# Performance work log

Measured on AMD Instinct MI355X. Metric: run time of the kernel, lower is better.

The kernel has to match this reference:

```python
import jax, jax.numpy as jnp
import numpy as np

B, N, D, C = 256, 256, 512, 1024
EPS = 1e-12  # F.normalize eps


def _l2norm(x):
    n = jnp.linalg.norm(x, axis=-1, keepdims=True)
    return x / jnp.maximum(n, EPS)


def setup_inputs() -> dict:
    key = jax.random.key(0)
    k1, k2, k3 = jax.random.split(key, 3)
    return {
        "image_tokens": jax.random.normal(k1, (B, N, D), dtype=jnp.float32),
        "text_features": jax.random.normal(k2, (C, D), dtype=jnp.float32),
        "log_tau": jnp.asarray(np.log(0.07), dtype=jnp.float32),
        "log_attn_tau": jnp.asarray(np.log(0.07), dtype=jnp.float32),
        "pid_labels": jax.random.randint(k3, (B,), 0, C),
    }


def reference(image_tokens, text_features, log_tau, log_attn_tau, pid_labels):
    toks = _l2norm(image_tokens.astype(jnp.float32))        # [B,N,D]
    txt = _l2norm(text_features.astype(jnp.float32))        # [C,D]
    sims = jnp.einsum('bnd,cd->bnc', toks, txt)             # [B,N,C]
    gt = pid_labels.astype(jnp.int32)
    # sims[arange(B), :, gt] -> [B,N]
    sims_gt = jnp.take_along_axis(sims, gt[:, None, None], axis=2)[..., 0]
    attn_tau = jnp.clip(jnp.exp(log_attn_tau), 0.01, 1.0)
    w = jax.nn.softmax(sims_gt / attn_tau, axis=1)          # [B,N]
    logits = jnp.einsum('bn,bnc->bc', w, sims)              # [B,C]
    tau = jnp.clip(jnp.exp(log_tau), 0.01, 1.0)
    logits = logits / tau
    # cross_entropy with label_smoothing=0.0, mean reduction
    logp = jax.nn.log_softmax(logits, axis=-1)
    nll = -jnp.take_along_axis(logp, gt[:, None], axis=1)[:, 0]
    return jnp.mean(nll)
```

## Files before the change

### kernel.cpp

```cpp
#include <hip/hip_runtime.h>
#include <math.h>

#define Bb 256
#define Nn 256
#define Dd 512
#define Cc 1024
#define KC 8
#define KD (Dd / KC)
#define BT 8

__device__ __forceinline__ float waveReduceSum(float v) {
    #pragma unroll
    for (int off = 32; off > 0; off >>= 1)
        v += __shfl_xor(v, off, 64);
    return v;
}
__device__ __forceinline__ float waveReduceMax(float v) {
    #pragma unroll
    for (int off = 32; off > 0; off >>= 1)
        v = fmaxf(v, __shfl_xor(v, off, 64));
    return v;
}

__global__ void __launch_bounds__(1024) k_attn_q(const float* __restrict__ toks,
                                                 const float* __restrict__ txt,
                                                 const int* __restrict__ pid,
                                                 const float* __restrict__ log_attn_tau,
                                                 float* __restrict__ q,
                                                 float* __restrict__ txt_t,
                                                 float* __restrict__ accf,
                                                 int* __restrict__ cnt) {
    const int b = blockIdx.x;
    const int tid = threadIdx.x;
    const int wv = tid >> 6;
    const int lane = tid & 63;
    __shared__ float xg[Dd];
    __shared__ float r8[8];
    __shared__ float tss[16];
    __shared__ float qpart_s[16][Dd];
    __shared__ float ms[16], Ss[16];

    if (b == 0 && tid == 0) { accf[0] = 0.0f; cnt[0] = 0; }

    const int g = pid[b];
    float v = 0.f;
    if (tid < Dd) v = txt[(size_t)g * Dd + tid];

    const int c0 = b * 4;
    const int row = tid >> 8;
    const int col2 = (tid & 255) * 2;
    const float2 tv = *(const float2*)&txt[(size_t)(c0 + row) * Dd + col2];

    float p = waveReduceSum(v * v);
    float ssp = waveReduceSum(tv.x * tv.x + tv.y * tv.y);
    if (lane == 0) { if (wv < 8) r8[wv] = p; tss[wv] = ssp; }
    __syncthreads();

    const float tot = r8[0]+r8[1]+r8[2]+r8[3]+r8[4]+r8[5]+r8[6]+r8[7];
    const float invg = 1.0f / fmaxf(sqrtf(tot), 1e-12f);
    if (tid < Dd) xg[tid] = v * invg;

    {
        const float rss = tss[4*row] + tss[4*row+1] + tss[4*row+2] + tss[4*row+3];
        const float invr = 1.0f / fmaxf(sqrtf(rss), 1e-12f);
        txt_t[(size_t)col2 * Cc + c0 + row] = tv.x * invr;
        txt_t[(size_t)(col2 + 1) * Cc + c0 + row] = tv.y * invr;
    }
    __syncthreads();

    float at = expf(log_attn_tau[0]);
    at = fminf(fmaxf(at, 0.01f), 1.0f);
    const float iat = 1.0f / at;

    const float4 xg0 = *(const float4*)&xg[lane * 8];
    const float4 xg1 = *(const float4*)&xg[lane * 8 + 4];

    float m = -INFINITY, S = 0.0f;
    float qa[8] = {0.f, 0.f, 0.f, 0.f, 0.f, 0.f, 0.f, 0.f};

    const float* base = toks + ((size_t)b * Nn + wv * 16) * Dd + (size_t)lane * 8;
    float4 c0v[4], c1v[4];
    #pragma unroll
    for (int k = 0; k < 4; ++k) {
        c0v[k] = *(const float4*)(base + k * Dd);
        c1v[k] = *(const float4*)(base + k * Dd + 4);
    }
    #pragma unroll
    for (int batch = 0; batch < 4; ++batch) {
        float4 n0[4], n1[4];
        if (batch < 3) {
            const float* pn = base + (batch + 1) * 4 * Dd;
            #pragma unroll
            for (int k = 0; k < 4; ++k) {
                n0[k] = *(const float4*)(pn + k * Dd);
                n1[k] = *(const float4*)(pn + k * Dd + 4);
            }
        }
        float dt[4], ss[4];
        #pragma unroll
        for (int k = 0; k < 4; ++k) {
            dt[k] = c0v[k].x*xg0.x + c0v[k].y*xg0.y + c0v[k].z*xg0.z + c0v[k].w*xg0.w
                  + c1v[k].x*xg1.x + c1v[k].y*xg1.y + c1v[k].z*xg1.z + c1v[k].w*xg1.w;
            ss[k] = c0v[k].x*c0v[k].x + c0v[k].y*c0v[k].y + c0v[k].z*c0v[k].z + c0v[k].w*c0v[k].w
                  + c1v[k].x*c1v[k].x + c1v[k].y*c1v[k].y + c1v[k].z*c1v[k].z + c1v[k].w*c1v[k].w;
        }
        #pragma unroll
        for (int off = 32; off > 0; off >>= 1) {
            #pragma unroll
            for (int k = 0; k < 4; ++k) {
                dt[k] += __shfl_xor(dt[k], off, 64);
                ss[k] += __shfl_xor(ss[k], off, 64);
            }
        }
        #pragma unroll
        for (int k = 0; k < 4; ++k) {
            const float inv = 1.0f / fmaxf(sqrtf(ss[k]), 1e-12f);
            const float s = dt[k] * inv;
            if (s > m) {
                const float sc = expf((m - s) * iat);
                S = S * sc + 1.0f;
                qa[0] = qa[0]*sc + inv*c0v[k].x; qa[1] = qa[1]*sc + inv*c0v[k].y;
                qa[2] = qa[2]*sc + inv*c0v[k].z; qa[3] = qa[3]*sc + inv*c0v[k].w;
                qa[4] = qa[4]*sc + inv*c1v[k].x; qa[5] = qa[5]*sc + inv*c1v[k].y;
                qa[6] = qa[6]*sc + inv*c1v[k].z; qa[7] = qa[7]*sc + inv*c1v[k].w;
                m = s;
            } else {
                const float e = expf((s - m) * iat);
                S += e;
                const float w = e * inv;
                qa[0] = fmaf(w, c0v[k].x, qa[0]); qa[1] = fmaf(w, c0v[k].y, qa[1]);
                qa[2] = fmaf(w, c0v[k].z, qa[2]); qa[3] = fmaf(w, c0v[k].w, qa[3]);
                qa[4] = fmaf(w, c1v[k].x, qa[4]); qa[5] = fmaf(w, c1v[k].y, qa[5]);
                qa[6] = fmaf(w, c1v[k].z, qa[6]); qa[7] = fmaf(w, c1v[k].w, qa[7]);
            }
        }
        #pragma unroll
        for (int k = 0; k < 4; ++k) { c0v[k] = n0[k]; c1v[k] = n1[k]; }
    }
    #pragma unroll
    for (int j = 0; j < 8; ++j) qpart_s[wv][lane * 8 + j] = qa[j];
    if (lane == 0) { ms[wv] = m; Ss[wv] = S; }
    __syncthreads();
    if (tid < Dd) {
        float M = -INFINITY;
        #pragma unroll
        for (int w = 0; w < 16; ++w) M = fmaxf(M, ms[w]);
        float Stot = 0.f, acc = 0.f;
        #pragma unroll
        for (int w = 0; w < 16; ++w) {
            const float sc = expf((ms[w] - M) * iat);
            Stot = fmaf(Ss[w], sc, Stot);
            acc = fmaf(qpart_s[w][tid], sc, acc);
        }
        q[(size_t)b * Dd + tid] = acc / Stot;
    }
}

__global__ void k_logits(const float* __restrict__ q, const float* __restrict__ txt_t,
                         float* __restrict__ part) {
    const int b0 = blockIdx.x * BT;
    const int kc = blockIdx.y;
    const int d0 = kc * KD;
    const int t = threadIdx.x;
    __shared__ float qs[BT][KD];
    for (int i = t; i < BT * KD; i += 256)
        qs[i >> 6][i & 63] = q[(size_t)(b0 + (i >> 6)) * Dd + d0 + (i & 63)];
    __syncthreads();
    const float4* xt = (const float4*)txt_t;
    float4 a[BT];
    #pragma unroll
    for (int j = 0; j < BT; ++j) a[j] = make_float4(0.f, 0.f, 0.f, 0.f);
    #pragma unroll 2
    for (int d = 0; d < KD; d += 4) {
        const float4 x0 = xt[(size_t)(d0 + d + 0) * (Cc / 4) + t];
        const float4 x1 = xt[(size_t)(d0 + d + 1) * (Cc / 4) + t];
        const float4 x2 = xt[(size_t)(d0 + d + 2) * (Cc / 4) + t];
        const float4 x3 = xt[(size_t)(d0 + d + 3) * (Cc / 4) + t];
        #pragma unroll
        for (int j = 0; j < BT; ++j) {
            const float4 qj = *(const float4*)&qs[j][d];
            a[j].x = fmaf(qj.x,x0.x,a[j].x); a[j].y = fmaf(qj.x,x0.y,a[j].y); a[j].z = fmaf(qj.x,x0.z,a[j].z); a[j].w = fmaf(qj.x,x0.w,a[j].w);
            a[j].x = fmaf(qj.y,x1.x,a[j].x); a[j].y = fmaf(qj.y,x1.y,a[j].y); a[j].z = fmaf(qj.y,x1.z,a[j].z); a[j].w = fmaf(qj.y,x1.w,a[j].w);
            a[j].x = fmaf(qj.z,x2.x,a[j].x); a[j].y = fmaf(qj.z,x2.y,a[j].y); a[j].z = fmaf(qj.z,x2.z,a[j].z); a[j].w = fmaf(qj.z,x2.w,a[j].w);
            a[j].x = fmaf(qj.w,x3.x,a[j].x); a[j].y = fmaf(qj.w,x3.y,a[j].y); a[j].z = fmaf(qj.w,x3.z,a[j].z); a[j].w = fmaf(qj.w,x3.w,a[j].w);
        }
    }
    float* pb = part + ((size_t)kc * Bb + b0) * Cc;
    #pragma unroll
    for (int j = 0; j < BT; ++j) ((float4*)(pb + (size_t)j * Cc))[t] = a[j];
}

__global__ void k_lse_mean(const float* __restrict__ part, const int* __restrict__ pid,
                           const float* __restrict__ log_tau,
                           float* __restrict__ accf, int* __restrict__ cnt,
                           float* __restrict__ out) {
    const int b = blockIdx.x;
    const int t = threadIdx.x;
    float4 l = {0,0,0,0};
    #pragma unroll
    for (int kc = 0; kc < KC; ++kc) {
        const float4 p = ((const float4*)(part + ((size_t)kc * Bb + b) * Cc))[t];
        l.x += p.x; l.y += p.y; l.z += p.z; l.w += p.w;
    }
    float tau = expf(log_tau[0]);
    tau = fminf(fmaxf(tau, 0.01f), 1.0f);
    const float itau = 1.0f / tau;
    l.x *= itau; l.y *= itau; l.z *= itau; l.w *= itau;

    const int g = pid[b];
    __shared__ float redm[4], reds[4], sgt;
    if ((g >> 2) == t) {
        const float v[4] = {l.x, l.y, l.z, l.w};
        sgt = v[g & 3];
    }
    float m = fmaxf(fmaxf(l.x, l.y), fmaxf(l.z, l.w));
    m = waveReduceMax(m);
    if ((t & 63) == 0) redm[t >> 6] = m;
    __syncthreads();
    m = fmaxf(fmaxf(redm[0], redm[1]), fmaxf(redm[2], redm[3]));
    float e = expf(l.x - m) + expf(l.y - m) + expf(l.z - m) + expf(l.w - m);
    e = waveReduceSum(e);
    if ((t & 63) == 0) reds[t >> 6] = e;
    __syncthreads();
    if (t == 0) {
        const float S = reds[0] + reds[1] + reds[2] + reds[3];
        const float my = (m + logf(S) - sgt) * (1.0f / (float)Bb);
        atomicAdd(accf, my);
        __threadfence();
        const int c = atomicAdd(cnt, 1);
        if (c == Bb - 1) {
            out[0] = atomicAdd(accf, 0.0f);
        }
    }
}

extern "C" void kernel_launch(void* const* d_in, const int* in_sizes, int n_in,
                              void* d_out, int out_size, void* d_ws, size_t ws_size,
                              hipStream_t stream) {
    const float* toks = (const float*)d_in[0];
    const float* txt = (const float*)d_in[1];
    const float* log_tau = (const float*)d_in[2];
    const float* log_attn_tau = (const float*)d_in[3];
    const int* pid = (const int*)d_in[4];
    float* out = (float*)d_out;

    float* ws = (float*)d_ws;
    float* txt_t = ws;
    float* q     = txt_t + (size_t)Dd * Cc;
    float* part  = q + (size_t)Bb * Dd;
    float* accf  = part + (size_t)KC * Bb * Cc;
    int*   cnt   = (int*)(accf + 1);

    k_attn_q<<<Bb, 1024, 0, stream>>>(toks, txt, pid, log_attn_tau, q, txt_t, accf, cnt);
    k_logits<<<dim3(Bb / BT, KC), 256, 0, stream>>>(q, txt_t, part);
    k_lse_mean<<<Bb, 256, 0, stream>>>(part, pid, log_tau, accf, cnt, out);
}
```

Before: 220.9 us.

## Fuse three kernels into one cooperative kernel with grid syncs

Measured after the change: 311.0 us. +40.8%, slower.

```diff
diff --git a/kernel.cpp b/kernel.cpp
--- a/kernel.cpp
+++ b/kernel.cpp
@@ -1,4 +1,5 @@
 #include <hip/hip_runtime.h>
+#include <hip/hip_cooperative_groups.h>
 #include <math.h>
 
 #define Bb 256
@@ -9,6 +10,8 @@
 #define KD (Dd / KC)
 #define BT 8
 
+namespace cg = cooperative_groups;
+
 __device__ __forceinline__ float waveReduceSum(float v) {
     #pragma unroll
     for (int off = 32; off > 0; off >>= 1)
@@ -22,215 +25,211 @@
     return v;
 }
 
-__global__ void __launch_bounds__(1024) k_attn_q(const float* __restrict__ toks,
-                                                 const float* __restrict__ txt,
-                                                 const int* __restrict__ pid,
-                                                 const float* __restrict__ log_attn_tau,
-                                                 float* __restrict__ q,
-                                                 float* __restrict__ txt_t,
-                                                 float* __restrict__ accf,
-                                                 int* __restrict__ cnt) {
-    const int b = blockIdx.x;
+__global__ void __launch_bounds__(1024, 1) k_fused(
+    const float* __restrict__ toks, const float* __restrict__ txt,
+    const int* __restrict__ pid, const float* __restrict__ log_attn_tau,
+    const float* __restrict__ log_tau,
+    float* __restrict__ q, float* __restrict__ txt_t,
+    float* __restrict__ part, float* __restrict__ nll, float* __restrict__ out)
+{
+    cg::grid_group grid = cg::this_grid();
+    const int bid = blockIdx.x;
     const int tid = threadIdx.x;
     const int wv = tid >> 6;
     const int lane = tid & 63;
+
     __shared__ float xg[Dd];
     __shared__ float r8[8];
     __shared__ float tss[16];
     __shared__ float qpart_s[16][Dd];
     __shared__ float ms[16], Ss[16];
-
-    if (b == 0 && tid == 0) { accf[0] = 0.0f; cnt[0] = 0; }
-
-    const int g = pid[b];
-    float v = 0.f;
-    if (tid < Dd) v = txt[(size_t)g * Dd + tid];
-
-    const int c0 = b * 4;
-    const int row = tid >> 8;
-    const int col2 = (tid & 255) * 2;
-    const float2 tv = *(const float2*)&txt[(size_t)(c0 + row) * Dd + col2];
-
-    float p = waveReduceSum(v * v);
-    float ssp = waveReduceSum(tv.x * tv.x + tv.y * tv.y);
-    if (lane == 0) { if (wv < 8) r8[wv] = p; tss[wv] = ssp; }
-    __syncthreads();
-
-    const float tot = r8[0]+r8[1]+r8[2]+r8[3]+r8[4]+r8[5]+r8[6]+r8[7];
-    const float invg = 1.0f / fmaxf(sqrtf(tot), 1e-12f);
-    if (tid < Dd) xg[tid] = v * invg;
+    __shared__ float sgt_s;
 
     {
-        const float rss = tss[4*row] + tss[4*row+1] + tss[4*row+2] + tss[4*row+3];
-        const float invr = 1.0f / fmaxf(sqrtf(rss), 1e-12f);
-        txt_t[(size_t)col2 * Cc + c0 + row] = tv.x * invr;
-        txt_t[(size_t)(col2 + 1) * Cc + c0 + row] = tv.y * invr;
-    }
-    __syncthreads();
-
-    float at = expf(log_attn_tau[0]);
-    at = fminf(fmaxf(at, 0.01f), 1.0f);
-    const float iat = 1.0f / at;
-
-    const float4 xg0 = *(const float4*)&xg[lane * 8];
-    const float4 xg1 = *(const float4*)&xg[lane * 8 + 4];
-
-    float m = -INFINITY, S = 0.0f;
-    float qa[8] = {0.f, 0.f, 0.f, 0.f, 0.f, 0.f, 0.f, 0.f};
-
-    const float* base = toks + ((size_t)b * Nn + wv * 16) * Dd + (size_t)lane * 8;
-    float4 c0v[4], c1v[4];
-    #pragma unroll
-    for (int k = 0; k < 4; ++k) {
-        c0v[k] = *(const float4*)(base + k * Dd);
-        c1v[k] = *(const float4*)(base + k * Dd + 4);
-    }
-    #pragma unroll
-    for (int batch = 0; batch < 4; ++batch) {
-        float4 n0[4], n1[4];
-        if (batch < 3) {
-            const float* pn = base + (batch + 1) * 4 * Dd;
+        const int b = bid;
+        const int g = pid[b];
+        float v = 0.f;
+        if (tid < Dd) v = txt[(size_t)g * Dd + tid];
+
+        const int c0 = b * 4;
+        const int row = tid >> 8;
+        const int col2 = (tid & 255) * 2;
+        const float2 tv = *(const float2*)&txt[(size_t)(c0 + row) * Dd + col2];
+
+        float p = waveReduceSum(v * v);
+        float ssp = waveReduceSum(tv.x * tv.x + tv.y * tv.y);
+        if (lane == 0) { if (wv < 8) r8[wv] = p; tss[wv] = ssp; }
+        __syncthreads();
+
+        const float tot = r8[0]+r8[1]+r8[2]+r8[3]+r8[4]+r8[5]+r8[6]+r8[7];
+        const float invg = 1.0f / fmaxf(sqrtf(tot), 1e-12f);
+        if (tid < Dd) xg[tid] = v * invg;
+
+        {
+            const float rss = tss[4*row] + tss[4*row+1] + tss[4*row+2] + tss[4*row+3];
+            const float invr = 1.0f / fmaxf(sqrtf(rss), 1e-12f);
+            txt_t[(size_t)col2 * Cc + c0 + row] = tv.x * invr;
+            txt_t[(size_t)(col2 + 1) * Cc + c0 + row] = tv.y * invr;
+        }
+        __syncthreads();
+
+        float at = expf(log_attn_tau[0]);
+        at = fminf(fmaxf(at, 0.01f), 1.0f);
+        const float iat = 1.0f / at;
+
+        const float4 xg0 = *(const float4*)&xg[lane * 8];
+        const float4 xg1 = *(const float4*)&xg[lane * 8 + 4];
+
+        float m = -INFINITY, S = 0.0f;
+        float qa[8] = {0.f, 0.f, 0.f, 0.f, 0.f, 0.f, 0.f, 0.f};
+
+        const float* base = toks + ((size_t)b * Nn + wv * 16) * Dd + (size_t)lane * 8;
+        float4 c0v[4], c1v[4];
+        #pragma unroll
+        for (int k = 0; k < 4; ++k) {
+            c0v[k] = *(const float4*)(base + k * Dd);
+            c1v[k] = *(const float4*)(base + k * Dd + 4);
+        }
+        #pragma unroll
+        for (int batch = 0; batch < 4; ++batch) {
+            float4 n0[4], n1[4];
+            if (batch < 3) {
+                const float* pn = base + (batch + 1) * 4 * Dd;
+                #pragma unroll
+                for (int k = 0; k < 4; ++k) {
+                    n0[k] = *(const float4*)(pn + k * Dd);
+                    n1[k] = *(const float4*)(pn + k * Dd + 4);
+                }
+            }
+            float dt[4], ss[4];
             #pragma unroll
             for (int k = 0; k < 4; ++k) {
-                n0[k] = *(const float4*)(pn + k * Dd);
-                n1[k] = *(const float4*)(pn + k * Dd + 4);
-            }
-        }
-        float dt[4], ss[4];
-        #pragma unroll
-        for (int k = 0; k < 4; ++k) {
-            dt[k] = c0v[k].x*xg0.x + c0v[k].y*xg0.y + c0v[k].z*xg0.z + c0v[k].w*xg0.w
-                  + c1v[k].x*xg1.x + c1v[k].y*xg1.y + c1v[k].z*xg1.z + c1v[k].w*xg1.w;
-            ss[k] = c0v[k].x*c0v[k].x + c0v[k].y*c0v[k].y + c0v[k].z*c0v[k].z + c0v[k].w*c0v[k].w
-                  + c1v[k].x*c1v[k].x + c1v[k].y*c1v[k].y + c1v[k].z*c1v[k].z + c1v[k].w*c1v[k].w;
-        }
-        #pragma unroll
-        for (int off = 32; off > 0; off >>= 1) {
+                dt[k] = c0v[k].x*xg0.x + c0v[k].y*xg0.y + c0v[k].z*xg0.z + c0v[k].w*xg0.w
+                      + c1v[k].x*xg1.x + c1v[k].y*xg1.y + c1v[k].z*xg1.z + c1v[k].w*xg1.w;
+                ss[k] = c0v[k].x*c0v[k].x + c0v[k].y*c0v[k].y + c0v[k].z*c0v[k].z + c0v[k].w*c0v[k].w
+                      + c1v[k].x*c1v[k].x + c1v[k].y*c1v[k].y + c1v[k].z*c1v[k].z + c1v[k].w*c1v[k].w;
+            }
+            #pragma unroll
+            for (int off = 32; off > 0; off >>= 1) {
+                #pragma unroll
+                for (int k = 0; k < 4; ++k) {
+                    dt[k] += __shfl_xor(dt[k], off, 64);
+                    ss[k] += __shfl_xor(ss[k], off, 64);
+                }
+            }
             #pragma unroll
             for (int k = 0; k < 4; ++k) {
-                dt[k] += __shfl_xor(dt[k], off, 64);
-                ss[k] += __shfl_xor(ss[k], off, 64);
-            }
-        }
-        #pragma unroll
-        for (int k = 0; k < 4; ++k) {
-            const float inv = 1.0f / fmaxf(sqrtf(ss[k]), 1e-12f);
-            const float s = dt[k] * inv;
-            if (s > m) {
-                const float sc = expf((m - s) * iat);
-                S = S * sc + 1.0f;
-                qa[0] = qa[0]*sc + inv*c0v[k].x; qa[1] = qa[1]*sc + inv*c0v[k].y;
-                qa[2] = qa[2]*sc + inv*c0v[k].z; qa[3] = qa[3]*sc + inv*c0v[k].w;
-                qa[4] = qa[4]*sc + inv*c1v[k].x; qa[5] = qa[5]*sc + inv*c1v[k].y;
-                qa[6] = qa[6]*sc + inv*c1v[k].z; qa[7] = qa[7]*sc + inv*c1v[k].w;
-                m = s;
-            } else {
-                const float e = expf((s - m) * iat);
-                S += e;
-                const float w = e * inv;
-                qa[0] = fmaf(w, c0v[k].x, qa[0]); qa[1] = fmaf(w, c0v[k].y, qa[1]);
-                qa[2] = fmaf(w, c0v[k].z, qa[2]); qa[3] = fmaf(w, c0v[k].w, qa[3]);
-                qa[4] = fmaf(w, c1v[k].x, qa[4]); qa[5] = fmaf(w, c1v[k].y, qa[5]);
-                qa[6] = fmaf(w, c1v[k].z, qa[6]); qa[7] = fmaf(w, c1v[k].w, qa[7]);
-            }
-        }
-        #pragma unroll
-        for (int k = 0; k < 4; ++k) { c0v[k] = n0[k]; c1v[k] = n1[k]; }
-    }
-    #pragma unroll
-    for (int j = 0; j < 8; ++j) qpart_s[wv][lane * 8 + j] = qa[j];
-    if (lane == 0) { ms[wv] = m; Ss[wv] = S; }
-    __syncthreads();
-    if (tid < Dd) {
+                const float inv = 1.0f / fmaxf(sqrtf(ss[k]), 1e-12f);
+                const float s = dt[k] * inv;
+                if (s > m) {
+                    const float sc = expf((m - s) * iat);
+                    S = S * sc + 1.0f;
+                    qa[0] = qa[0]*sc + inv*c0v[k].x; qa[1] = qa[1]*sc + inv*c0v[k].y;
+                    qa[2] = qa[2]*sc + inv*c0v[k].z; qa[3] = qa[3]*sc + inv*c0v[k].w;
+                    qa[4] = qa[4]*sc + inv*c1v[k].x; qa[5] = qa[5]*sc + inv*c1v[k].y;
+                    qa[6] = qa[6]*sc + inv*c1v[k].z; qa[7] = qa[7]*sc + inv*c1v[k].w;
+                    m = s;
+                } else {
+                    const float e = expf((s - m) * iat);
+                    S += e;
+                    const float w = e * inv;
+                    qa[0] = fmaf(w, c0v[k].x, qa[0]); qa[1] = fmaf(w, c0v[k].y, qa[1]);
+                    qa[2] = fmaf(w, c0v[k].z, qa[2]); qa[3] = fmaf(w, c0v[k].w, qa[3]);
+                    qa[4] = fmaf(w, c1v[k].x, qa[4]); qa[5] = fmaf(w, c1v[k].y, qa[5]);
+                    qa[6] = fmaf(w, c1v[k].z, qa[6]); qa[7] = fmaf(w, c1v[k].w, qa[7]);
+                }
+            }
+            #pragma unroll
+            for (int k = 0; k < 4; ++k) { c0v[k] = n0[k]; c1v[k] = n1[k]; }
+        }
+        #pragma unroll
+        for (int j = 0; j < 8; ++j) qpart_s[wv][lane * 8 + j] = qa[j];
+        if (lane == 0) { ms[wv] = m; Ss[wv] = S; }
+        __syncthreads();
+        if (tid < Dd) {
+            float M = -INFINITY;
+            #pragma unroll
+            for (int w = 0; w < 16; ++w) M = fmaxf(M, ms[w]);
+            float Stot = 0.f, acc = 0.f;
+            #pragma unroll
+            for (int w = 0; w < 16; ++w) {
+                const float sc = expf((ms[w] - M) * iat);
+                Stot = fmaf(Ss[w], sc, Stot);
+                acc = fmaf(qpart_s[w][tid], sc, acc);
+            }
+            q[(size_t)b * Dd + tid] = acc / Stot;
+        }
+    }
+
+    grid.sync();
+
+    {
+        const int kc = bid >> 5;
+        const int b0 = (bid & 31) * BT;
+        const int d0 = kc * KD;
+        float* qs = xg;
+        if (tid < BT * KD)
+            qs[tid] = q[(size_t)(b0 + (tid >> 6)) * Dd + d0 + (tid & 63)];
+        __syncthreads();
+        const int c = tid;
+        float a[BT];
+        #pragma unroll
+        for (int j = 0; j < BT; ++j) a[j] = 0.f;
+        #pragma unroll 8
+        for (int d = 0; d < KD; ++d) {
+            const float x = txt_t[(size_t)(d0 + d) * Cc + c];
+            #pragma unroll
+            for (int j = 0; j < BT; ++j)
+                a[j] = fmaf(qs[j * KD + d], x, a[j]);
+        }
+        float* pb = part + ((size_t)kc * Bb + b0) * Cc + c;
+        #pragma unroll
+        for (int j = 0; j < BT; ++j) pb[(size_t)j * Cc] = a[j];
+    }
+
+    grid.sync();
+
+    {
+        const int b = bid;
+        float l = 0.f;
+        #pragma unroll
+        for (int kc2 = 0; kc2 < KC; ++kc2)
+            l += part[((size_t)kc2 * Bb + b) * Cc + tid];
+        float tau = expf(log_tau[0]);
+        tau = fminf(fmaxf(tau, 0.01f), 1.0f);
+        l *= (1.0f / tau);
+
+        const int g = pid[b];
+        if (tid == g) sgt_s = l;
+        float m = waveReduceMax(l);
+        if (lane == 0) ms[wv] = m;
+        __syncthreads();
         float M = -INFINITY;
         #pragma unroll
         for (int w = 0; w < 16; ++w) M = fmaxf(M, ms[w]);
-        float Stot = 0.f, acc = 0.f;
-        #pragma unroll
-        for (int w = 0; w < 16; ++w) {
-            const float sc = expf((ms[w] - M) * iat);
-            Stot = fmaf(Ss[w], sc, Stot);
-            acc = fmaf(qpart_s[w][tid], sc, acc);
-        }
-        q[(size_t)b * Dd + tid] = acc / Stot;
-    }
-}
-
-__global__ void k_logits(const float* __restrict__ q, const float* __restrict__ txt_t,
-                         float* __restrict__ part) {
-    const int b0 = blockIdx.x * BT;
-    const int kc = blockIdx.y;
-    const int d0 = kc * KD;
-    const int t = threadIdx.x;
-    __shared__ float qs[BT][KD];
-    for (int i = t; i < BT * KD; i += 256)
-        qs[i >> 6][i & 63] = q[(size_t)(b0 + (i >> 6)) * Dd + d0 + (i & 63)];
-    __syncthreads();
-    const float4* xt = (const float4*)txt_t;
-    float4 a[BT];
-    #pragma unroll
-    for (int j = 0; j < BT; ++j) a[j] = make_float4(0.f, 0.f, 0.f, 0.f);
-    #pragma unroll 2
-    for (int d = 0; d < KD; d += 4) {
-        const float4 x0 = xt[(size_t)(d0 + d + 0) * (Cc / 4) + t];
-        const float4 x1 = xt[(size_t)(d0 + d + 1) * (Cc / 4) + t];
-        const float4 x2 = xt[(size_t)(d0 + d + 2) * (Cc / 4) + t];
-        const float4 x3 = xt[(size_t)(d0 + d + 3) * (Cc / 4) + t];
-        #pragma unroll
-        for (int j = 0; j < BT; ++j) {
-            const float4 qj = *(const float4*)&qs[j][d];
-            a[j].x = fmaf(qj.x,x0.x,a[j].x); a[j].y = fmaf(qj.x,x0.y,a[j].y); a[j].z = fmaf(qj.x,x0.z,a[j].z); a[j].w = fmaf(qj.x,x0.w,a[j].w);
-            a[j].x = fmaf(qj.y,x1.x,a[j].x); a[j].y = fmaf(qj.y,x1.y,a[j].y); a[j].z = fmaf(qj.y,x1.z,a[j].z); a[j].w = fmaf(qj.y,x1.w,a[j].w);
-            a[j].x = fmaf(qj.z,x2.x,a[j].x); a[j].y = fmaf(qj.z,x2.y,a[j].y); a[j].z = fmaf(qj.z,x2.z,a[j].z); a[j].w = fmaf(qj.z,x2.w,a[j].w);
-            a[j].x = fmaf(qj.w,x3.x,a[j].x); a[j].y = fmaf(qj.w,x3.y,a[j].y); a[j].z = fmaf(qj.w,x3.z,a[j].z); a[j].w = fmaf(qj.w,x3.w,a[j].w);
-        }
-    }
-    float* pb = part + ((size_t)kc * Bb + b0) * Cc;
-    #pragma unroll
-    for (int j = 0; j < BT; ++j) ((float4*)(pb + (size_t)j * Cc))[t] = a[j];
-}
-
-__global__ void k_lse_mean(const float* __restrict__ part, const int* __restrict__ pid,
-                           const float* __restrict__ log_tau,
-                           float* __restrict__ accf, int* __restrict__ cnt,
-                           float* __restrict__ out) {
-    const int b = blockIdx.x;
-    const int t = threadIdx.x;
-    float4 l = {0,0,0,0};
-    #pragma unroll
-    for (int kc = 0; kc < KC; ++kc) {
-        const float4 p = ((const float4*)(part + ((size_t)kc * Bb + b) * Cc))[t];
-        l.x += p.x; l.y += p.y; l.z += p.z; l.w += p.w;
-    }
-    float tau = expf(log_tau[0]);
-    tau = fminf(fmaxf(tau, 0.01f), 1.0f);
-    const float itau = 1.0f / tau;
-    l.x *= itau; l.y *= itau; l.z *= itau; l.w *= itau;
-
-    const int g = pid[b];
-    __shared__ float redm[4], reds[4], sgt;
-    if ((g >> 2) == t) {
-        const float v[4] = {l.x, l.y, l.z, l.w};
-        sgt = v[g & 3];
-    }
-    float m = fmaxf(fmaxf(l.x, l.y), fmaxf(l.z, l.w));
-    m = waveReduceMax(m);
-    if ((t & 63) == 0) redm[t >> 6] = m;
-    __syncthreads();
-    m = fmaxf(fmaxf(redm[0], redm[1]), fmaxf(redm[2], redm[3]));
-    float e = expf(l.x - m) + expf(l.y - m) + expf(l.z - m) + expf(l.w - m);
-    e = waveReduceSum(e);
-    if ((t & 63) == 0) reds[t >> 6] = e;
-    __syncthreads();
-    if (t == 0) {
-        const float S = reds[0] + reds[1] + reds[2] + reds[3];
-        const float my = (m + logf(S) - sgt) * (1.0f / (float)Bb);
-        atomicAdd(accf, my);
-        __threadfence();
-        const int c = atomicAdd(cnt, 1);
-        if (c == Bb - 1) {
-            out[0] = atomicAdd(accf, 0.0f);
-        }
+        float e = expf(l - M);
+        e = waveReduceSum(e);
+        if (lane == 0) Ss[wv] = e;
+        __syncthreads();
+        if (tid == 0) {
+            float S = 0.f;
+            #pragma unroll
+            for (int w = 0; w < 16; ++w) S += Ss[w];
+            nll[b] = M + logf(S) - sgt_s;
+        }
+    }
+
+    grid.sync();
+
+    if (bid == 0) {
+        float v = 0.f;
+        if (tid < Bb) v = nll[tid];
+        if (tid < Bb) {
+            v = waveReduceSum(v);
+            if (lane == 0) r8[wv] = v;
+        }
+        __syncthreads();
+        if (tid == 0) out[0] = (r8[0] + r8[1] + r8[2] + r8[3]) * (1.0f / (float)Bb);
     }
 }
 
@@ -248,10 +247,10 @@
     float* txt_t = ws;
     float* q     = txt_t + (size_t)Dd * Cc;
     float* part  = q + (size_t)Bb * Dd;
-    float* accf  = part + (size_t)KC * Bb * Cc;
-    int*   cnt   = (int*)(accf + 1);
-
-    k_attn_q<<<Bb, 1024, 0, stream>>>(toks, txt, pid, log_attn_tau, q, txt_t, accf, cnt);
-    k_logits<<<dim3(Bb / BT, KC), 256, 0, stream>>>(q, txt_t, part);
-    k_lse_mean<<<Bb, 256, 0, stream>>>(part, pid, log_tau, accf, cnt, out);
-}
+    float* nll   = part + (size_t)KC * Bb * Cc;
+
+    void* args[] = {(void*)&toks, (void*)&txt, (void*)&pid, (void*)&log_attn_tau,
+                    (void*)&log_tau, (void*)&q, (void*)&txt_t, (void*)&part,
+                    (void*)&nll, (void*)&out};
+    hipLaunchCooperativeKernel((void*)k_fused, dim3(Bb), dim3(1024), args, 0, stream);
+}
```

## Split attention pass into 1024 smaller blocks and merge partials in logits kernel

Applied to the files above, without the earlier changes.

Result: slower. 226.0 us (+2.3%).

```diff
diff --git a/kernel.cpp b/kernel.cpp
--- a/kernel.cpp
+++ b/kernel.cpp
@@ -8,6 +8,8 @@
 #define KC 8
 #define KD (Dd / KC)
 #define BT 8
+#define NS 4
+#define NW 16
 
 __device__ __forceinline__ float waveReduceSum(float v) {
     #pragma unroll
@@ -22,50 +24,36 @@
     return v;
 }
 
-__global__ void __launch_bounds__(1024) k_attn_q(const float* __restrict__ toks,
-                                                 const float* __restrict__ txt,
-                                                 const int* __restrict__ pid,
-                                                 const float* __restrict__ log_attn_tau,
-                                                 float* __restrict__ q,
-                                                 float* __restrict__ txt_t,
-                                                 float* __restrict__ accf,
-                                                 int* __restrict__ cnt) {
-    const int b = blockIdx.x;
+__global__ void __launch_bounds__(256, 8) k_attn_part(
+    const float* __restrict__ toks, const float* __restrict__ txt,
+    const int* __restrict__ pid, const float* __restrict__ log_attn_tau,
+    float* __restrict__ txt_t, float* __restrict__ pq,
+    float* __restrict__ pm, float* __restrict__ pS,
+    float* __restrict__ accf, int* __restrict__ cnt)
+{
+    const int blk = blockIdx.x;
+    const int b = blk >> 2, s = blk & 3;
     const int tid = threadIdx.x;
-    const int wv = tid >> 6;
-    const int lane = tid & 63;
+    const int wv = tid >> 6, lane = tid & 63;
     __shared__ float xg[Dd];
-    __shared__ float r8[8];
-    __shared__ float tss[16];
-    __shared__ float qpart_s[16][Dd];
-    __shared__ float ms[16], Ss[16];
-
-    if (b == 0 && tid == 0) { accf[0] = 0.0f; cnt[0] = 0; }
-
+    __shared__ float red_g[4], red_c[4];
+
+    if (blk == 0 && tid == 0) { accf[0] = 0.0f; cnt[0] = 0; }
+
+    const int c = blk;
     const int g = pid[b];
-    float v = 0.f;
-    if (tid < Dd) v = txt[(size_t)g * Dd + tid];
-
-    const int c0 = b * 4;
-    const int row = tid >> 8;
-    const int col2 = (tid & 255) * 2;
-    const float2 tv = *(const float2*)&txt[(size_t)(c0 + row) * Dd + col2];
-
-    float p = waveReduceSum(v * v);
-    float ssp = waveReduceSum(tv.x * tv.x + tv.y * tv.y);
-    if (lane == 0) { if (wv < 8) r8[wv] = p; tss[wv] = ssp; }
-    __syncthreads();
-
-    const float tot = r8[0]+r8[1]+r8[2]+r8[3]+r8[4]+r8[5]+r8[6]+r8[7];
-    const float invg = 1.0f / fmaxf(sqrtf(tot), 1e-12f);
-    if (tid < Dd) xg[tid] = v * invg;
-
-    {
-        const float rss = tss[4*row] + tss[4*row+1] + tss[4*row+2] + tss[4*row+3];
-        const float invr = 1.0f / fmaxf(sqrtf(rss), 1e-12f);
-        txt_t[(size_t)col2 * Cc + c0 + row] = tv.x * invr;
-        txt_t[(size_t)(col2 + 1) * Cc + c0 + row] = tv.y * invr;
-    }
+    const float2 gv = *(const float2*)&txt[(size_t)g * Dd + tid * 2];
+    const float2 cv = *(const float2*)&txt[(size_t)c * Dd + tid * 2];
+    const float pg = waveReduceSum(gv.x * gv.x + gv.y * gv.y);
+    const float pc = waveReduceSum(cv.x * cv.x + cv.y * cv.y);
+    if (lane == 0) { red_g[wv] = pg; red_c[wv] = pc; }
+    __syncthreads();
+    const float invg = 1.0f / fmaxf(sqrtf(red_g[0]+red_g[1]+red_g[2]+red_g[3]), 1e-12f);
+    const float invc = 1.0f / fmaxf(sqrtf(red_c[0]+red_c[1]+red_c[2]+red_c[3]), 1e-12f);
+    xg[tid * 2]     = gv.x * invg;
+    xg[tid * 2 + 1] = gv.y * invg;
+    txt_t[(size_t)(tid * 2) * Cc + c]     = cv.x * invc;
+    txt_t[(size_t)(tid * 2 + 1) * Cc + c] = cv.y * invc;
     __syncthreads();
 
     float at = expf(log_attn_tau[0]);
@@ -78,27 +66,19 @@
     float m = -INFINITY, S = 0.0f;
     float qa[8] = {0.f, 0.f, 0.f, 0.f, 0.f, 0.f, 0.f, 0.f};
 
-    const float* base = toks + ((size_t)b * Nn + wv * 16) * Dd + (size_t)lane * 8;
-    float4 c0v[4], c1v[4];
-    #pragma unroll
-    for (int k = 0; k < 4; ++k) {
-        c0v[k] = *(const float4*)(base + k * Dd);
-        c1v[k] = *(const float4*)(base + k * Dd + 4);
-    }
-    #pragma unroll
-    for (int batch = 0; batch < 4; ++batch) {
-        float4 n0[4], n1[4];
-        if (batch < 3) {
-            const float* pn = base + (batch + 1) * 4 * Dd;
-            #pragma unroll
-            for (int k = 0; k < 4; ++k) {
-                n0[k] = *(const float4*)(pn + k * Dd);
-                n1[k] = *(const float4*)(pn + k * Dd + 4);
-            }
-        }
-        float dt[4], ss[4];
-        #pragma unroll
-        for (int k = 0; k < 4; ++k) {
+    const float* base = toks + ((size_t)b * Nn + s * 64 + wv * 16) * Dd + (size_t)lane * 8;
+    #pragma unroll
+    for (int batch = 0; batch < 8; ++batch) {
+        float4 c0v[2], c1v[2];
+        #pragma unroll
+        for (int k = 0; k < 2; ++k) {
+            const float* p = base + (size_t)(batch * 2 + k) * Dd;
+            c0v[k] = *(const float4*)p;
+            c1v[k] = *(const float4*)(p + 4);
+        }
+        float dt[2], ss[2];
+        #pragma unroll
+        for (int k = 0; k < 2; ++k) {
             dt[k] = c0v[k].x*xg0.x + c0v[k].y*xg0.y + c0v[k].z*xg0.z + c0v[k].w*xg0.w
                   + c1v[k].x*xg1.x + c1v[k].y*xg1.y + c1v[k].z*xg1.z + c1v[k].w*xg1.w;
             ss[k] = c0v[k].x*c0v[k].x + c0v[k].y*c0v[k].y + c0v[k].z*c0v[k].z + c0v[k].w*c0v[k].w
@@ -107,25 +87,25 @@
         #pragma unroll
         for (int off = 32; off > 0; off >>= 1) {
             #pragma unroll
-            for (int k = 0; k < 4; ++k) {
+            for (int k = 0; k < 2; ++k) {
                 dt[k] += __shfl_xor(dt[k], off, 64);
                 ss[k] += __shfl_xor(ss[k], off, 64);
             }
         }
         #pragma unroll
-        for (int k = 0; k < 4; ++k) {
+        for (int k = 0; k < 2; ++k) {
             const float inv = 1.0f / fmaxf(sqrtf(ss[k]), 1e-12f);
-            const float s = dt[k] * inv;
-            if (s > m) {
-                const float sc = expf((m - s) * iat);
+            const float sv = dt[k] * inv;
+            if (sv > m) {
+                const float sc = expf((m - sv) * iat);
                 S = S * sc + 1.0f;
                 qa[0] = qa[0]*sc + inv*c0v[k].x; qa[1] = qa[1]*sc + inv*c0v[k].y;
                 qa[2] = qa[2]*sc + inv*c0v[k].z; qa[3] = qa[3]*sc + inv*c0v[k].w;
                 qa[4] = qa[4]*sc + inv*c1v[k].x; qa[5] = qa[5]*sc + inv*c1v[k].y;
                 qa[6] = qa[6]*sc + inv*c1v[k].z; qa[7] = qa[7]*sc + inv*c1v[k].w;
-                m = s;
+                m = sv;
             } else {
-                const float e = expf((s - m) * iat);
+                const float e = expf((sv - m) * iat);
                 S += e;
                 const float w = e * inv;
                 qa[0] = fmaf(w, c0v[k].x, qa[0]); qa[1] = fmaf(w, c0v[k].y, qa[1]);
@@ -134,38 +114,45 @@
                 qa[6] = fmaf(w, c1v[k].z, qa[6]); qa[7] = fmaf(w, c1v[k].w, qa[7]);
             }
         }
-        #pragma unroll
-        for (int k = 0; k < 4; ++k) { c0v[k] = n0[k]; c1v[k] = n1[k]; }
-    }
-    #pragma unroll
-    for (int j = 0; j < 8; ++j) qpart_s[wv][lane * 8 + j] = qa[j];
-    if (lane == 0) { ms[wv] = m; Ss[wv] = S; }
-    __syncthreads();
-    if (tid < Dd) {
-        float M = -INFINITY;
-        #pragma unroll
-        for (int w = 0; w < 16; ++w) M = fmaxf(M, ms[w]);
-        float Stot = 0.f, acc = 0.f;
-        #pragma unroll
-        for (int w = 0; w < 16; ++w) {
-            const float sc = expf((ms[w] - M) * iat);
-            Stot = fmaf(Ss[w], sc, Stot);
-            acc = fmaf(qpart_s[w][tid], sc, acc);
-        }
-        q[(size_t)b * Dd + tid] = acc / Stot;
-    }
-}
-
-__global__ void k_logits(const float* __restrict__ q, const float* __restrict__ txt_t,
-                         float* __restrict__ part) {
+    }
+    const int ws = s * 4 + wv;
+    float* pqw = pq + ((size_t)b * NW + ws) * Dd + lane * 8;
+    #pragma unroll
+    for (int j = 0; j < 8; ++j) pqw[j] = qa[j];
+    if (lane == 0) { pm[b * NW + ws] = m; pS[b * NW + ws] = S; }
+}
+
+__global__ void k_logits(const float* __restrict__ pq, const float* __restrict__ pm,
+                         const float* __restrict__ pS, const float* __restrict__ log_attn_tau,
+                         const float* __restrict__ txt_t, float* __restrict__ part)
+{
     const int b0 = blockIdx.x * BT;
     const int kc = blockIdx.y;
     const int d0 = kc * KD;
     const int t = threadIdx.x;
     __shared__ float qs[BT][KD];
-    for (int i = t; i < BT * KD; i += 256)
-        qs[i >> 6][i & 63] = q[(size_t)(b0 + (i >> 6)) * Dd + d0 + (i & 63)];
-    __syncthreads();
+
+    float at = expf(log_attn_tau[0]);
+    at = fminf(fmaxf(at, 0.01f), 1.0f);
+    const float iat = 1.0f / at;
+
+    for (int slot = t; slot < BT * KD; slot += 256) {
+        const int j = slot >> 6, d = slot & 63;
+        const int b = b0 + j;
+        float M = -INFINITY;
+        #pragma unroll
+        for (int w = 0; w < NW; ++w) M = fmaxf(M, pm[b * NW + w]);
+        float Stot = 0.f, acc = 0.f;
+        #pragma unroll
+        for (int w = 0; w < NW; ++w) {
+            const float sc = expf((pm[b * NW + w] - M) * iat);
+            Stot = fmaf(pS[b * NW + w], sc, Stot);
+            acc = fmaf(sc, pq[((size_t)b * NW + w) * Dd + d0 + d], acc);
+        }
+        qs[j][d] = acc / Stot;
+    }
+    __syncthreads();
+
     const float4* xt = (const float4*)txt_t;
     float4 a[BT];
     #pragma unroll
@@ -246,12 +233,15 @@
 
     float* ws = (float*)d_ws;
     float* txt_t = ws;
-    float* q     = txt_t + (size_t)Dd * Cc;
-    float* part  = q + (size_t)Bb * Dd;
+    float* pq    = txt_t + (size_t)Dd * Cc;
+    float* pm    = pq + (size_t)Bb * NW * Dd;
+    float* pS    = pm + (size_t)Bb * NW;
+    float* part  = pS + (size_t)Bb * NW;
     float* accf  = part + (size_t)KC * Bb * Cc;
     int*   cnt   = (int*)(accf + 1);
 
-    k_attn_q<<<Bb, 1024, 0, stream>>>(toks, txt, pid, log_attn_tau, q, txt_t, accf, cnt);
-    k_logits<<<dim3(Bb / BT, KC), 256, 0, stream>>>(q, txt_t, part);
+    k_attn_part<<<Bb * NS, 256, 0, stream>>>(toks, txt, pid, log_attn_tau,
+                                             txt_t, pq, pm, pS, accf, cnt);
+    k_logits<<<dim3(Bb / BT, KC), 256, 0, stream>>>(pq, pm, pS, log_attn_tau, txt_t, part);
     k_lse_mean<<<Bb, 256, 0, stream>>>(part, pid, log_tau, accf, cnt, out);
 }
```
